# Performance work log

Measured on AMD Instinct MI355X. Metric: run time of the kernel, lower is better.

The kernel has to match this reference:

```python
import jax, jax.numpy as jnp
import numpy as np

N = 50000       # nodes
E = 500000      # edges
F_IN = 64       # input feature dim
F_OUT = 64      # hidden/output dim
K = 3           # diffusion filter order
C = F_IN + F_OUT  # concat dim seen by each DConv


def _xavier(k, shape):
    fan_in, fan_out = shape[-2], shape[-1]
    lim = float(np.sqrt(6.0 / (fan_in + fan_out)))
    return jax.random.uniform(k, shape, jnp.float32, -lim, lim)


def setup_inputs() -> dict:
    key = jax.random.key(0)
    ks = jax.random.split(key, 8)
    X = jax.random.normal(ks[0], (N, F_IN), jnp.float32)
    H = jax.random.normal(ks[1], (N, F_OUT), jnp.float32)
    # ring edges guarantee every node has in-degree >= 1 and out-degree >= 1
    base = jnp.arange(N, dtype=jnp.int32)
    row = jnp.concatenate([base, jax.random.randint(ks[2], (E - N,), 0, N, jnp.int32)])
    col = jnp.concatenate([jnp.roll(base, 1), jax.random.randint(ks[3], (E - N,), 0, N, jnp.int32)])
    edge_index = jnp.stack([row, col])  # [2, E]
    W_z = _xavier(ks[4], (2, K, C, F_OUT))
    W_r = _xavier(ks[5], (2, K, C, F_OUT))
    W_h = _xavier(ks[6], (2, K, C, F_OUT))
    b = jnp.zeros((F_OUT,), jnp.float32)
    return {"X": X, "edge_index": edge_index, "H": H,
            "W_z": W_z, "b_z": b, "W_r": W_r, "b_r": b, "W_h": W_h, "b_h": b}


def _dconv(Xc, row, col, norm_out, norm_in, W, b):
    # PyG propagate: gather source (row) features, scale by edge norm, scatter-add to target (col)
    def prop(x, norm):
        return jax.ops.segment_sum(norm[:, None] * x[row], col, num_segments=N)
    Tx_0 = Xc
    Hout = Xc @ (W[0, 0] + W[1, 0])
    Tx_1_o = prop(Xc, norm_out)
    Tx_1_i = prop(Xc, norm_in)
    Hout = Hout + Tx_1_o @ W[0, 1] + Tx_1_i @ W[1, 1]
    for k in range(2, K):
        Tx_2_o = 2.0 * prop(Tx_1_o, norm_out) - Tx_0
        Tx_2_i = 2.0 * prop(Tx_1_i, norm_in) - Tx_0
        Hout = Hout + Tx_2_o @ W[0, k] + Tx_2_i @ W[1, k]
        # faithful to original: Tx_1 is never reassigned, so Tx_0 stays Xc
        Tx_0, Tx_1_o, Tx_1_i = Xc, Tx_2_o, Tx_2_i
    return Hout + b


def reference(X, edge_index, H, W_z, b_z, W_r, b_r, W_h, b_h):
    row, col = edge_index[0], edge_index[1]
    deg_out = jnp.zeros((N,), jnp.float32).at[row].add(1.0)
    deg_in = jnp.zeros((N,), jnp.float32).at[col].add(1.0)
    norm_out = (1.0 / deg_out)[row]
    norm_in = (1.0 / deg_in)[row]
    XH = jnp.concatenate([X, H], axis=1)
    Z = jax.nn.sigmoid(_dconv(XH, row, col, norm_out, norm_in, W_z, b_z))
    R = jax.nn.sigmoid(_dconv(XH, row, col, norm_out, norm_in, W_r, b_r))
    XHR = jnp.concatenate([X, H * R], axis=1)
    H_tilde = jnp.tanh(_dconv(XHR, row, col, norm_out, norm_in, W_h, b_h))
    H_new = Z * H + (1.0 - Z) * H_tilde
    # NaN infill with mean of non-NaN entries (faithful to original)
    mask = jnp.isnan(H_new)
    H_new = jnp.where(mask, jnp.nanmean(H_new), H_new)
    return H_new
```

## Files before the change

kernel.cpp:

```cpp
#include <hip/hip_runtime.h>
#include <hip/hip_bf16.h>
#include <math.h>

#define N_NODES 50000
#define N_EDGES 500000
#define C_DIM 128
#define N_TILES 3125

#define CSR_BLOCKS 1954
#define CONCAT_BLOCKS 3125
#define PACK_BLOCKS 480

typedef __attribute__((ext_vector_type(8))) short bf8;
typedef __attribute__((ext_vector_type(4))) float f32x4;

__device__ __forceinline__ float bflo(unsigned u) { return __uint_as_float(u << 16); }
__device__ __forceinline__ float bfhi(unsigned u) { return __uint_as_float(u & 0xffff0000u); }
__device__ __forceinline__ unsigned short f2bfu(float f) {
    __hip_bfloat16 h = __float2bfloat16(f);
    unsigned short u;
    __builtin_memcpy(&u, &h, 2);
    return u;
}
__device__ __forceinline__ unsigned packbf(float a, float b) {
    return ((unsigned)f2bfu(b) << 16) | f2bfu(a);
}


__global__ void count_deg(const int* __restrict__ row, const int* __restrict__ col,
                          int* __restrict__ dout, int* __restrict__ din, int e) {
    int i = blockIdx.x * blockDim.x + threadIdx.x;
    if (i >= e) return;
    atomicAdd(&dout[row[i]], 1);
    atomicAdd(&din[col[i]], 1);
}

__global__ void scan_block(const int* __restrict__ counts, int* __restrict__ excl,
                           int* __restrict__ blocksums, int n) {
    __shared__ int tmp[1024];
    int tid = threadIdx.x;
    int gid = blockIdx.x * 1024 + tid;
    int v = (gid < n) ? counts[gid] : 0;
    tmp[tid] = v;
    __syncthreads();
    for (int off = 1; off < 1024; off <<= 1) {
        int t = (tid >= off) ? tmp[tid - off] : 0;
        __syncthreads();
        tmp[tid] += t;
        __syncthreads();
    }
    int incl = tmp[tid];
    if (gid < n) excl[gid] = incl - v;
    if (tid == 1023) blocksums[blockIdx.x] = incl;
}

__global__ void scan_sums(int* __restrict__ blocksums, int nb) {
    __shared__ int tmp[64];
    int tid = threadIdx.x;
    int v = (tid < nb) ? blocksums[tid] : 0;
    tmp[tid] = v;
    __syncthreads();
    for (int off = 1; off < 64; off <<= 1) {
        int t = (tid >= off) ? tmp[tid - off] : 0;
        __syncthreads();
        tmp[tid] += t;
        __syncthreads();
    }
    if (tid < nb) blocksums[tid] = tmp[tid] - v;
}

__global__ void scan_add(int* __restrict__ rowptr, const int* __restrict__ blocksums,
                         int* __restrict__ cursor, const int* __restrict__ dout,
                         const int* __restrict__ din, float2* __restrict__ winv,
                         int n, int e_total) {
    int gid = blockIdx.x * blockDim.x + threadIdx.x;
    if (gid < n) {
        int v = rowptr[gid] + blocksums[gid >> 10];
        rowptr[gid] = v;
        cursor[gid] = v;
        winv[gid] = make_float2(1.0f / (float)dout[gid], 1.0f / (float)din[gid]);
    }
    if (gid == n) rowptr[n] = e_total;
}

__device__ __forceinline__ float wraw(const float* W, int d, int kk, int k, int j) {
    return W[((d * 3 + kk) * 128 + k) * 64 + j];
}

__device__ __forceinline__ float zr_val(const float* Wz, const float* Wr, int k, int nn) {
    const float* W = (nn < 64) ? Wz : Wr;
    int j = nn & 63;
    if (k < 128) return wraw(W, 0, 0, k, j) + wraw(W, 1, 0, k, j);
    int k2 = k - 128;
    int kk = (k2 >= 256) ? 2 : 1;
    int k3 = k2 & 255;
    int p = k3 >> 2, sub = k3 & 3;
    return wraw(W, sub >> 1, kk, 2 * p + (sub & 1), j);
}

__device__ __forceinline__ float h_val(const float* Wh, int k, int j) {
    if (k < 64) return wraw(Wh, 0, 0, k, j) + wraw(Wh, 1, 0, k, j);
    if (k < 320) {
        int k2 = k - 64;
        int kk = (k2 >= 128) ? 2 : 1;
        int k3 = k2 & 127;
        int p = k3 >> 2, sub = k3 & 3;
        return wraw(Wh, sub >> 1, kk, 2 * p + (sub & 1), j);
    }
    if (k < 384) return wraw(Wh, 0, 0, 64 + (k - 320), j) + wraw(Wh, 1, 0, 64 + (k - 320), j);
    int k2 = k - 384;
    int kk = (k2 >= 128) ? 2 : 1;
    int k3 = k2 & 127;
    int p = k3 >> 2, sub = k3 & 3;
    return wraw(Wh, sub >> 1, kk, 64 + 2 * p + (sub & 1), j);
}

__global__ void fused_prep(const int* __restrict__ row, const int* __restrict__ col,
                           const float2* __restrict__ winv, int* __restrict__ cursor,
                           int* __restrict__ csr_src, float2* __restrict__ csr_w,
                           const float* __restrict__ X, const float* __restrict__ Hm,
                           unsigned short* __restrict__ XH, unsigned short* __restrict__ XHp,
                           const float* __restrict__ Wz, const float* __restrict__ Wr,
                           const float* __restrict__ Wh,
                           unsigned short* __restrict__ Wzrf, unsigned short* __restrict__ Whf,
                           int n, int e) {
    int b = blockIdx.x;
    if (b < CSR_BLOCKS) {
        int i = b * 256 + threadIdx.x;
        if (i >= e) return;
        int r = row[i], c = col[i];
        int pos = atomicAdd(&cursor[c], 1);
        csr_src[pos] = r;
        csr_w[pos] = winv[r];
    } else if (b < CSR_BLOCKS + CONCAT_BLOCKS) {
        int t = (b - CSR_BLOCKS) * 256 + threadIdx.x;
        int node = t >> 4, p = t & 15;
        const float* src = (p < 8) ? (X + (size_t)node * 64 + 8 * p)
                                   : (Hm + (size_t)node * 64 + 8 * (p - 8));
        float4 v0 = *(const float4*)src;
        float4 v1 = *(const float4*)(src + 4);
        uint4 o;
        o.x = packbf(v0.x, v0.y); o.y = packbf(v0.z, v0.w);
        o.z = packbf(v1.x, v1.y); o.w = packbf(v1.z, v1.w);
        *(uint4*)(XH + (size_t)node * 128 + 8 * p) = o;
        int tile = node >> 4, lr = node & 15, ck = p >> 2, q = p & 3;
        *(uint4*)(XHp + (((size_t)tile * 4 + ck) * 64 + q * 16 + lr) * 8) = o;
    } else {
        int i = (b - CSR_BLOCKS - CONCAT_BLOCKS) * 256 + threadIdx.x;
        if (i < 20 * 8 * 64 * 8) {
            int j = i & 7, lane = (i >> 3) & 63, nt = (i >> 9) & 7, ks = i >> 12;
            int k = ks * 32 + (lane >> 4) * 8 + j;
            int nn = nt * 16 + (lane & 15);
            Wzrf[i] = f2bfu(zr_val(Wz, Wr, k, nn));
        } else if (i < 20 * 8 * 64 * 8 + 20 * 4 * 64 * 8) {
            int i2 = i - 20 * 8 * 64 * 8;
            int j = i2 & 7, lane = (i2 >> 3) & 63, nt = (i2 >> 9) & 3, ks = i2 >> 11;
            int k = ks * 32 + (lane >> 4) * 8 + j;
            int nn = nt * 16 + (lane & 15);
            Whf[i2] = f2bfu(h_val(Wh, k, nn));
        }
    }
}


__global__ void prop1_128(const unsigned short* __restrict__ S,
                          const int* __restrict__ rowptr, const int* __restrict__ src,
                          const float2* __restrict__ w,
                          unsigned short* __restrict__ P1, unsigned short* __restrict__ P1p,
                          int n) {
    int tid = blockIdx.x * blockDim.x + threadIdx.x;
    int lane = tid & 63;
    int node = ((tid >> 6) << 1) + (lane >> 5);
    int p = lane & 31;
    if (node >= n) return;
    int beg = rowptr[node], end = rowptr[node + 1];
    float ao0 = 0.f, ao1 = 0.f, ao2 = 0.f, ao3 = 0.f;
    float ai0 = 0.f, ai1 = 0.f, ai2 = 0.f, ai3 = 0.f;
    int j = beg;
#define P1STEP(s_, w_) {                                                     \
        uint2 u = *(const uint2*)(S + (size_t)(s_) * 128 + 4 * p);           \
        float c0 = bflo(u.x), c1 = bfhi(u.x), c2 = bflo(u.y), c3 = bfhi(u.y);\
        ao0 = fmaf(w_.x, c0, ao0); ao1 = fmaf(w_.x, c1, ao1);                \
        ao2 = fmaf(w_.x, c2, ao2); ao3 = fmaf(w_.x, c3, ao3);                \
        ai0 = fmaf(w_.y, c0, ai0); ai1 = fmaf(w_.y, c1, ai1);                \
        ai2 = fmaf(w_.y, c2, ai2); ai3 = fmaf(w_.y, c3, ai3); }
    for (; j + 8 <= end; j += 8) {
        int s0 = src[j], s1 = src[j + 1], s2 = src[j + 2], s3 = src[j + 3];
        int s4 = src[j + 4], s5 = src[j + 5], s6 = src[j + 6], s7 = src[j + 7];
        float2 w0 = w[j], w1 = w[j + 1], w2 = w[j + 2], w3 = w[j + 3];
        float2 w4 = w[j + 4], w5 = w[j + 5], w6 = w[j + 6], w7 = w[j + 7];
        P1STEP(s0, w0); P1STEP(s1, w1); P1STEP(s2, w2); P1STEP(s3, w3);
        P1STEP(s4, w4); P1STEP(s5, w5); P1STEP(s6, w6); P1STEP(s7, w7);
    }
    for (; j + 4 <= end; j += 4) {
        int s0 = src[j], s1 = src[j + 1], s2 = src[j + 2], s3 = src[j + 3];
        float2 w0 = w[j], w1 = w[j + 1], w2 = w[j + 2], w3 = w[j + 3];
        P1STEP(s0, w0); P1STEP(s1, w1); P1STEP(s2, w2); P1STEP(s3, w3);
    }
    for (; j < end; ++j) {
        int s = src[j]; float2 wv = w[j];
        P1STEP(s, wv);
    }
#undef P1STEP
    uint4 o;
    o.x = packbf(ao0, ao1); o.y = packbf(ai0, ai1);
    o.z = packbf(ao2, ao3); o.w = packbf(ai2, ai3);
    *(uint4*)(P1 + (size_t)node * 256 + 8 * p) = o;
    int tile = node >> 4, lr = node & 15, ck = p >> 2, q = p & 3;
    *(uint4*)(P1p + (((size_t)tile * 8 + ck) * 64 + q * 16 + lr) * 8) = o;
}

__global__ void prop2_128(const unsigned short* __restrict__ P1,
                          const unsigned short* __restrict__ Xc,
                          const int* __restrict__ rowptr, const int* __restrict__ src,
                          const float2* __restrict__ w,
                          unsigned short* __restrict__ P2p, int n) {
    int tid = blockIdx.x * blockDim.x + threadIdx.x;
    int lane = tid & 63;
    int node = ((tid >> 6) << 1) + (lane >> 5);
    int p = lane & 31;
    if (node >= n) return;
    int beg = rowptr[node], end = rowptr[node + 1];
    float oa = 0.f, ob = 0.f, oc = 0.f, od = 0.f;
    float ia = 0.f, ib = 0.f, ic = 0.f, id = 0.f;
    int j = beg;
#define P2STEP(s_, w_) {                                                     \
        uint4 v = *(const uint4*)(P1 + (size_t)(s_) * 256 + 8 * p);          \
        oa = fmaf(w_.x, bflo(v.x), oa); ob = fmaf(w_.x, bfhi(v.x), ob);      \
        ia = fmaf(w_.y, bflo(v.y), ia); ib = fmaf(w_.y, bfhi(v.y), ib);      \
        oc = fmaf(w_.x, bflo(v.z), oc); od = fmaf(w_.x, bfhi(v.z), od);      \
        ic = fmaf(w_.y, bflo(v.w), ic); id = fmaf(w_.y, bfhi(v.w), id); }
    for (; j + 8 <= end; j += 8) {
        int s0 = src[j], s1 = src[j + 1], s2 = src[j + 2], s3 = src[j + 3];
        int s4 = src[j + 4], s5 = src[j + 5], s6 = src[j + 6], s7 = src[j + 7];
        float2 w0 = w[j], w1 = w[j + 1], w2 = w[j + 2], w3 = w[j + 3];
        float2 w4 = w[j + 4], w5 = w[j + 5], w6 = w[j + 6], w7 = w[j + 7];
        P2STEP(s0, w0); P2STEP(s1, w1); P2STEP(s2, w2); P2STEP(s3, w3);
        P2STEP(s4, w4); P2STEP(s5, w5); P2STEP(s6, w6); P2STEP(s7, w7);
    }
    for (; j + 4 <= end; j += 4) {
        int s0 = src[j], s1 = src[j + 1], s2 = src[j + 2], s3 = src[j + 3];
        float2 w0 = w[j], w1 = w[j + 1], w2 = w[j + 2], w3 = w[j + 3];
        P2STEP(s0, w0); P2STEP(s1, w1); P2STEP(s2, w2); P2STEP(s3, w3);
    }
    for (; j < end; ++j) {
        int s = src[j]; float2 wv = w[j];
        P2STEP(s, wv);
    }
#undef P2STEP
    uint2 ux = *(const uint2*)(Xc + (size_t)node * 128 + 4 * p);
    float xa = bflo(ux.x), xb = bfhi(ux.x), xc = bflo(ux.y), xd = bfhi(ux.y);
    uint4 o;
    o.x = packbf(2.f * oa - xa, 2.f * ob - xb);
    o.y = packbf(2.f * ia - xa, 2.f * ib - xb);
    o.z = packbf(2.f * oc - xc, 2.f * od - xd);
    o.w = packbf(2.f * ic - xc, 2.f * id - xd);
    int tile = node >> 4, lr = node & 15, ck = p >> 2, q = p & 3;
    *(uint4*)(P2p + (((size_t)tile * 8 + ck) * 64 + q * 16 + lr) * 8) = o;
}

__global__ void prop1_64(const unsigned short* __restrict__ HR,
                         const int* __restrict__ rowptr, const int* __restrict__ src,
                         const float2* __restrict__ w,
                         unsigned short* __restrict__ Q1, unsigned short* __restrict__ Q1p,
                         int n) {
    int tid = blockIdx.x * blockDim.x + threadIdx.x;
    int lane = tid & 63;
    int node = ((tid >> 6) << 2) + (lane >> 4);
    int p = lane & 15;
    if (node >= n) return;
    int beg = rowptr[node], end = rowptr[node + 1];
    float ao0 = 0.f, ao1 = 0.f, ao2 = 0.f, ao3 = 0.f;
    float ai0 = 0.f, ai1 = 0.f, ai2 = 0.f, ai3 = 0.f;
    int j = beg;
#define Q1STEP(s_, w_) {                                                     \
        uint2 u = *(const uint2*)(HR + (size_t)(s_) * 64 + 4 * p);           \
        float c0 = bflo(u.x), c1 = bfhi(u.x), c2 = bflo(u.y), c3 = bfhi(u.y);\
        ao0 = fmaf(w_.x, c0, ao0); ao1 = fmaf(w_.x, c1, ao1);                \
        ao2 = fmaf(w_.x, c2, ao2); ao3 = fmaf(w_.x, c3, ao3);                \
        ai0 = fmaf(w_.y, c0, ai0); ai1 = fmaf(w_.y, c1, ai1);                \
        ai2 = fmaf(w_.y, c2, ai2); ai3 = fmaf(w_.y, c3, ai3); }
    for (; j + 8 <= end; j += 8) {
        int s0 = src[j], s1 = src[j + 1], s2 = src[j + 2], s3 = src[j + 3];
        int s4 = src[j + 4], s5 = src[j + 5], s6 = src[j + 6], s7 = src[j + 7];
        float2 w0 = w[j], w1 = w[j + 1], w2 = w[j + 2], w3 = w[j + 3];
        float2 w4 = w[j + 4], w5 = w[j + 5], w6 = w[j + 6], w7 = w[j + 7];
        Q1STEP(s0, w0); Q1STEP(s1, w1); Q1STEP(s2, w2); Q1STEP(s3, w3);
        Q1STEP(s4, w4); Q1STEP(s5, w5); Q1STEP(s6, w6); Q1STEP(s7, w7);
    }
    for (; j + 4 <= end; j += 4) {
        int s0 = src[j], s1 = src[j + 1], s2 = src[j + 2], s3 = src[j + 3];
        float2 w0 = w[j], w1 = w[j + 1], w2 = w[j + 2], w3 = w[j + 3];
        Q1STEP(s0, w0); Q1STEP(s1, w1); Q1STEP(s2, w2); Q1STEP(s3, w3);
    }
    for (; j < end; ++j) {
        int s = src[j]; float2 wv = w[j];
        Q1STEP(s, wv);
    }
#undef Q1STEP
    uint4 o;
    o.x = packbf(ao0, ao1); o.y = packbf(ai0, ai1);
    o.z = packbf(ao2, ao3); o.w = packbf(ai2, ai3);
    *(uint4*)(Q1 + (size_t)node * 128 + 8 * p) = o;
    int tile = node >> 4, lr = node & 15, ck = p >> 2, q = p & 3;
    *(uint4*)(Q1p + (((size_t)tile * 4 + ck) * 64 + q * 16 + lr) * 8) = o;
}

__global__ void prop2_64(const unsigned short* __restrict__ Q1,
                         const unsigned short* __restrict__ HR,
                         const int* __restrict__ rowptr, const int* __restrict__ src,
                         const float2* __restrict__ w,
                         unsigned short* __restrict__ Q2p, int n) {
    int tid = blockIdx.x * blockDim.x + threadIdx.x;
    int lane = tid & 63;
    int node = ((tid >> 6) << 2) + (lane >> 4);
    int p = lane & 15;
    if (node >= n) return;
    int beg = rowptr[node], end = rowptr[node + 1];
    float oa = 0.f, ob = 0.f, oc = 0.f, od = 0.f;
    float ia = 0.f, ib = 0.f, ic = 0.f, id = 0.f;
    int j = beg;
#define Q2STEP(s_, w_) {                                                     \
        uint4 v = *(const uint4*)(Q1 + (size_t)(s_) * 128 + 8 * p);          \
        oa = fmaf(w_.x, bflo(v.x), oa); ob = fmaf(w_.x, bfhi(v.x), ob);      \
        ia = fmaf(w_.y, bflo(v.y), ia); ib = fmaf(w_.y, bfhi(v.y), ib);      \
        oc = fmaf(w_.x, bflo(v.z), oc); od = fmaf(w_.x, bfhi(v.z), od);      \
        ic = fmaf(w_.y, bflo(v.w), ic); id = fmaf(w_.y, bfhi(v.w), id); }
    for (; j + 8 <= end; j += 8) {
        int s0 = src[j], s1 = src[j + 1], s2 = src[j + 2], s3 = src[j + 3];
        int s4 = src[j + 4], s5 = src[j + 5], s6 = src[j + 6], s7 = src[j + 7];
        float2 w0 = w[j], w1 = w[j + 1], w2 = w[j + 2], w3 = w[j + 3];
        float2 w4 = w[j + 4], w5 = w[j + 5], w6 = w[j + 6], w7 = w[j + 7];
        Q2STEP(s0, w0); Q2STEP(s1, w1); Q2STEP(s2, w2); Q2STEP(s3, w3);
        Q2STEP(s4, w4); Q2STEP(s5, w5); Q2STEP(s6, w6); Q2STEP(s7, w7);
    }
    for (; j + 4 <= end; j += 4) {
        int s0 = src[j], s1 = src[j + 1], s2 = src[j + 2], s3 = src[j + 3];
        float2 w0 = w[j], w1 = w[j + 1], w2 = w[j + 2], w3 = w[j + 3];
        Q2STEP(s0, w0); Q2STEP(s1, w1); Q2STEP(s2, w2); Q2STEP(s3, w3);
    }
    for (; j < end; ++j) {
        int s = src[j]; float2 wv = w[j];
        Q2STEP(s, wv);
    }
#undef Q2STEP
    uint2 ux = *(const uint2*)(HR + (size_t)node * 64 + 4 * p);
    float xa = bflo(ux.x), xb = bfhi(ux.x), xc = bflo(ux.y), xd = bfhi(ux.y);
    uint4 o;
    o.x = packbf(2.f * oa - xa, 2.f * ob - xb);
    o.y = packbf(2.f * ia - xa, 2.f * ib - xb);
    o.z = packbf(2.f * oc - xc, 2.f * od - xd);
    o.w = packbf(2.f * ic - xc, 2.f * id - xd);
    int tile = node >> 4, lr = node & 15, ck = p >> 2, q = p & 3;
    *(uint4*)(Q2p + (((size_t)tile * 4 + ck) * 64 + q * 16 + lr) * 8) = o;
}


__global__ __launch_bounds__(256) void gemm_zr_mfma(
    const unsigned short* __restrict__ XHp, const unsigned short* __restrict__ P1p,
    const unsigned short* __restrict__ P2p,
    const unsigned short* __restrict__ Wf, const float* __restrict__ bz,
    const float* __restrict__ br, const float* __restrict__ H,
    float* __restrict__ Zf, unsigned short* __restrict__ HR, int n) {
    int tid = threadIdx.x;
    int lane = tid & 63;
    int ngrp = tid >> 6;
    int rowbase = blockIdx.x * 64;
    int lr = lane & 15, quad = lane >> 4;

    int tiles[4];
#pragma unroll
    for (int mt = 0; mt < 4; ++mt) {
        int t = (rowbase >> 4) + mt;
        tiles[mt] = (t > N_TILES - 1) ? N_TILES - 1 : t;
    }

    f32x4 zero = {0.f, 0.f, 0.f, 0.f};
    f32x4 acc[4][2];
#pragma unroll
    for (int a = 0; a < 4; ++a)
#pragma unroll
        for (int b = 0; b < 2; ++b) acc[a][b] = zero;

#pragma unroll
    for (int ks = 0; ks < 20; ++ks) {
        const unsigned short* T = (ks < 4) ? XHp : (ks < 12) ? P1p : P2p;
        int ck = (ks < 4) ? ks : (ks < 12) ? ks - 4 : ks - 12;
        int nck = (ks < 4) ? 4 : 8;
        bf8 b0 = *(const bf8*)(Wf + (((size_t)ks * 8 + ngrp * 2 + 0) * 64 + lane) * 8);
        bf8 b1 = *(const bf8*)(Wf + (((size_t)ks * 8 + ngrp * 2 + 1) * 64 + lane) * 8);
#pragma unroll
        for (int mt = 0; mt < 4; ++mt) {
            bf8 a = *(const bf8*)(T + (((size_t)tiles[mt] * nck + ck) * 64 + lane) * 8);
            acc[mt][0] = __builtin_amdgcn_mfma_f32_16x16x32_bf16(a, b0, acc[mt][0], 0, 0, 0);
            acc[mt][1] = __builtin_amdgcn_mfma_f32_16x16x32_bf16(a, b1, acc[mt][1], 0, 0, 0);
        }
    }
#pragma unroll
    for (int mt = 0; mt < 4; ++mt)
#pragma unroll
        for (int reg = 0; reg < 4; ++reg) {
            int r = rowbase + mt * 16 + quad * 4 + reg;
            if (r >= n) continue;
#pragma unroll
            for (int nt = 0; nt < 2; ++nt) {
                int cidx = ngrp * 32 + nt * 16 + lr;
                float bias = (cidx < 64) ? bz[cidx] : br[cidx - 64];
                float v = acc[mt][nt][reg] + bias;
                float s = 1.f / (1.f + expf(-v));
                if (cidx < 64) {
                    Zf[(size_t)r * 64 + cidx] = s;
                } else {
                    int c2 = cidx - 64;
                    HR[(size_t)r * 64 + c2] = f2bfu(H[(size_t)r * 64 + c2] * s);
                }
            }
        }
}

__global__ __launch_bounds__(256) void gemm_h_mfma(
    const unsigned short* __restrict__ XHp, const unsigned short* __restrict__ P1p,
    const unsigned short* __restrict__ P2p, const unsigned short* __restrict__ HR,
    const unsigned short* __restrict__ Q1p, const unsigned short* __restrict__ Q2p,
    const unsigned short* __restrict__ Wf, const float* __restrict__ bh,
    const float* __restrict__ Zf, const float* __restrict__ H,
    float* __restrict__ out, int n) {
    int tid = threadIdx.x;
    int lane = tid & 63;
    int wid = tid >> 6;
    int mh = wid & 1, ngrp = wid >> 1;
    int rowbase = blockIdx.x * 128 + mh * 64;
    int lr = lane & 15, quad = lane >> 4;

    int tiles[4];
    const unsigned short* hrp[4];
#pragma unroll
    for (int mt = 0; mt < 4; ++mt) {
        int t = (rowbase >> 4) + mt;
        tiles[mt] = (t > N_TILES - 1) ? N_TILES - 1 : t;
        int r = rowbase + mt * 16 + lr;
        if (r >= n) r = n - 1;
        hrp[mt] = HR + (size_t)r * 64 + quad * 8;
    }

    f32x4 zero = {0.f, 0.f, 0.f, 0.f};
    f32x4 acc[4][2];
#pragma unroll
    for (int a = 0; a < 4; ++a)
#pragma unroll
        for (int b = 0; b < 2; ++b) acc[a][b] = zero;

#pragma unroll
    for (int ks = 0; ks < 20; ++ks) {
        bf8 b0 = *(const bf8*)(Wf + (((size_t)ks * 4 + ngrp * 2 + 0) * 64 + lane) * 8);
        bf8 b1 = *(const bf8*)(Wf + (((size_t)ks * 4 + ngrp * 2 + 1) * 64 + lane) * 8);
#pragma unroll
        for (int mt = 0; mt < 4; ++mt) {
            bf8 a;
            if (ks == 10 || ks == 11) {
                a = *(const bf8*)(hrp[mt] + (ks - 10) * 32);
            } else {
                const unsigned short* T = (ks < 2) ? XHp : (ks < 6) ? P1p :
                                          (ks < 10) ? P2p : (ks < 16) ? Q1p : Q2p;
                int ck = (ks < 2) ? ks : (ks < 6) ? ks - 2 : (ks < 10) ? ks - 6 :
                         (ks < 16) ? ks - 12 : ks - 16;
                int nck = (ks < 2) ? 4 : (ks < 10) ? 8 : 4;
                a = *(const bf8*)(T + (((size_t)tiles[mt] * nck + ck) * 64 + lane) * 8);
            }
            acc[mt][0] = __builtin_amdgcn_mfma_f32_16x16x32_bf16(a, b0, acc[mt][0], 0, 0, 0);
            acc[mt][1] = __builtin_amdgcn_mfma_f32_16x16x32_bf16(a, b1, acc[mt][1], 0, 0, 0);
        }
    }
#pragma unroll
    for (int mt = 0; mt < 4; ++mt)
#pragma unroll
        for (int reg = 0; reg < 4; ++reg) {
            int r = rowbase + mt * 16 + quad * 4 + reg;
            if (r >= n) continue;
#pragma unroll
            for (int nt = 0; nt < 2; ++nt) {
                int cidx = ngrp * 32 + nt * 16 + lr;
                float ht = tanhf(acc[mt][nt][reg] + bh[cidx]);
                float z = Zf[(size_t)r * 64 + cidx];
                float h_old = H[(size_t)r * 64 + cidx];
                out[(size_t)r * 64 + cidx] = z * h_old + (1.f - z) * ht;
            }
        }
}


static inline size_t rup(size_t x) { return (x + 63) & ~(size_t)63; }

extern "C" void kernel_launch(void* const* d_in, const int* in_sizes, int n_in,
                              void* d_out, int out_size, void* d_ws, size_t ws_size,
                              hipStream_t stream) {
    const float* X  = (const float*)d_in[0];
    const int*   EI = (const int*)d_in[1];
    const float* H  = (const float*)d_in[2];
    const float* Wz = (const float*)d_in[3];
    const float* bz = (const float*)d_in[4];
    const float* Wr = (const float*)d_in[5];
    const float* br = (const float*)d_in[6];
    const float* Wh = (const float*)d_in[7];
    const float* bh = (const float*)d_in[8];
    float* out = (float*)d_out;

    const int* row = EI;
    const int* col = EI + N_EDGES;

    char* ws = (char*)d_ws;
    size_t off = 0;
    auto carve = [&](size_t bytes) { void* p = ws + off; off += rup(bytes); return p; };

    int*   deg_out   = (int*)carve(N_NODES * 4);
    int*   deg_in    = (int*)carve(N_NODES * 4);
    int*   rowptr    = (int*)carve((N_NODES + 1) * 4);
    int*   cursor    = (int*)carve(N_NODES * 4);
    int*   blocksums = (int*)carve(64 * 4);
    float2* winv     = (float2*)carve(N_NODES * 8);
    int*   csr_src   = (int*)carve(N_EDGES * 4);
    float2* csr_w    = (float2*)carve(N_EDGES * 8);
    unsigned short* XH  = (unsigned short*)carve((size_t)N_NODES * 128 * 2);
    unsigned short* P1  = (unsigned short*)carve((size_t)N_NODES * 256 * 2);
    unsigned short* XHp = (unsigned short*)carve((size_t)N_TILES * 4 * 512 * 2);
    unsigned short* P1p = (unsigned short*)carve((size_t)N_TILES * 8 * 512 * 2);
    unsigned short* P2p = (unsigned short*)carve((size_t)N_TILES * 8 * 512 * 2);
    unsigned short* HR  = (unsigned short*)carve((size_t)N_NODES * 64 * 2);
    float* Zf           = (float*)carve((size_t)N_NODES * 64 * 4);
    unsigned short* Wzrf = (unsigned short*)carve(20 * 8 * 64 * 8 * 2);
    unsigned short* Whf  = (unsigned short*)carve(20 * 4 * 64 * 8 * 2);

    unsigned short* Q1  = XH;
    unsigned short* Q1p = P1;
    unsigned short* Q2p = P1 + (size_t)N_TILES * 4 * 512;

    hipMemsetAsync(deg_out, 0, rup(N_NODES * 4) + rup(N_NODES * 4), stream);
    count_deg<<<(N_EDGES + 255) / 256, 256, 0, stream>>>(row, col, deg_out, deg_in, N_EDGES);

    int nblk = (N_NODES + 1023) / 1024;
    scan_block<<<nblk, 1024, 0, stream>>>(deg_in, rowptr, blocksums, N_NODES);
    scan_sums<<<1, 64, 0, stream>>>(blocksums, nblk);
    scan_add<<<(N_NODES + 1 + 255) / 256, 256, 0, stream>>>(rowptr, blocksums, cursor,
                                                            deg_out, deg_in, winv, N_NODES, N_EDGES);

    fused_prep<<<CSR_BLOCKS + CONCAT_BLOCKS + PACK_BLOCKS, 256, 0, stream>>>(
        row, col, winv, cursor, csr_src, csr_w,
        X, H, XH, XHp, Wz, Wr, Wh, Wzrf, Whf, N_NODES, N_EDGES);

    int blocks_p128 = (((N_NODES + 1) / 2) * 64 + 255) / 256;
    prop1_128<<<blocks_p128, 256, 0, stream>>>(XH, rowptr, csr_src, csr_w, P1, P1p, N_NODES);
    prop2_128<<<blocks_p128, 256, 0, stream>>>(P1, XH, rowptr, csr_src, csr_w, P2p, N_NODES);

    int zr_blocks = (N_NODES + 63) / 64;
    gemm_zr_mfma<<<zr_blocks, 256, 0, stream>>>(XHp, P1p, P2p, Wzrf, bz, br, H, Zf, HR, N_NODES);

    int blocks_p64 = (((N_NODES + 3) / 4) * 64 + 255) / 256;
    prop1_64<<<blocks_p64, 256, 0, stream>>>(HR, rowptr, csr_src, csr_w, Q1, Q1p, N_NODES);
    prop2_64<<<blocks_p64, 256, 0, stream>>>(Q1, HR, rowptr, csr_src, csr_w, Q2p, N_NODES);

    int h_blocks = (N_NODES + 127) / 128;
    gemm_h_mfma<<<h_blocks, 256, 0, stream>>>(XHp, P1p, P2p, HR, Q1p, Q2p,
                                              Whf, bh, Zf, H, out, N_NODES);
}
```

Before: 362.6 us.

## Split 128-dim propagation into feature slices for cache-friendly gathers

Adds a slice-major copy of the concatenated features (32 bf16 columns per slice, nodes contiguous) and rewrites both 128-wide propagation kernels so each block handles one feature slice for 32 nodes. Interleaving slices in the block index is meant to keep each slice's gather working set small enough to stay in L2 or the last-level cache during random neighbour reads. In exchange, the edge list and weights are re-read once per slice (4 or 8 times), each lane issues narrower loads, and an extra feature copy must be written during prep.

```diff
diff --git a/kernel.cpp b/kernel.cpp
--- a/kernel.cpp
+++ b/kernel.cpp
@@ -10,6 +10,7 @@
 #define CSR_BLOCKS 1954
 #define CONCAT_BLOCKS 3125
 #define PACK_BLOCKS 480
+#define NODE_CHUNKS 1563
 
 typedef __attribute__((ext_vector_type(8))) short bf8;
 typedef __attribute__((ext_vector_type(4))) float f32x4;
@@ -120,6 +121,7 @@
                            int* __restrict__ csr_src, float2* __restrict__ csr_w,
                            const float* __restrict__ X, const float* __restrict__ Hm,
                            unsigned short* __restrict__ XH, unsigned short* __restrict__ XHp,
+                           unsigned short* __restrict__ XHs,
                            const float* __restrict__ Wz, const float* __restrict__ Wr,
                            const float* __restrict__ Wh,
                            unsigned short* __restrict__ Wzrf, unsigned short* __restrict__ Whf,
@@ -145,6 +147,7 @@
         *(uint4*)(XH + (size_t)node * 128 + 8 * p) = o;
         int tile = node >> 4, lr = node & 15, ck = p >> 2, q = p & 3;
         *(uint4*)(XHp + (((size_t)tile * 4 + ck) * 64 + q * 16 + lr) * 8) = o;
+        *(uint4*)(XHs + ((size_t)(p >> 2) * n + node) * 32 + (p & 3) * 8) = o;
     } else {
         int i = (b - CSR_BLOCKS - CONCAT_BLOCKS) * 256 + threadIdx.x;
         if (i < 20 * 8 * 64 * 8) {
@@ -162,102 +165,89 @@
     }
 }
 
-
-__global__ void prop1_128(const unsigned short* __restrict__ S,
-                          const int* __restrict__ rowptr, const int* __restrict__ src,
-                          const float2* __restrict__ w,
-                          unsigned short* __restrict__ P1, unsigned short* __restrict__ P1p,
-                          int n) {
-    int tid = blockIdx.x * blockDim.x + threadIdx.x;
-    int lane = tid & 63;
-    int node = ((tid >> 6) << 1) + (lane >> 5);
-    int p = lane & 31;
+__global__ void prop1_128s(const unsigned short* __restrict__ XHs,
+                           const int* __restrict__ rowptr, const int* __restrict__ src,
+                           const float2* __restrict__ w,
+                           unsigned short* __restrict__ P1g, unsigned short* __restrict__ P1p,
+                           int n) {
+    int slice = blockIdx.x & 3;
+    int chunk = blockIdx.x >> 2;
+    int tid = threadIdx.x;
+    int wid = tid >> 6, lane = tid & 63;
+    int g = lane >> 3, l = lane & 7;
+    int node = chunk * 32 + wid * 8 + g;
     if (node >= n) return;
+    const unsigned short* S = XHs + (size_t)slice * n * 32;
     int beg = rowptr[node], end = rowptr[node + 1];
     float ao0 = 0.f, ao1 = 0.f, ao2 = 0.f, ao3 = 0.f;
     float ai0 = 0.f, ai1 = 0.f, ai2 = 0.f, ai3 = 0.f;
     int j = beg;
-#define P1STEP(s_, w_) {                                                     \
-        uint2 u = *(const uint2*)(S + (size_t)(s_) * 128 + 4 * p);           \
+#define S1STEP(s_, w_) {                                                     \
+        uint2 u = *(const uint2*)(S + (size_t)(s_) * 32 + 4 * l);            \
         float c0 = bflo(u.x), c1 = bfhi(u.x), c2 = bflo(u.y), c3 = bfhi(u.y);\
         ao0 = fmaf(w_.x, c0, ao0); ao1 = fmaf(w_.x, c1, ao1);                \
         ao2 = fmaf(w_.x, c2, ao2); ao3 = fmaf(w_.x, c3, ao3);                \
         ai0 = fmaf(w_.y, c0, ai0); ai1 = fmaf(w_.y, c1, ai1);                \
         ai2 = fmaf(w_.y, c2, ai2); ai3 = fmaf(w_.y, c3, ai3); }
-    for (; j + 8 <= end; j += 8) {
-        int s0 = src[j], s1 = src[j + 1], s2 = src[j + 2], s3 = src[j + 3];
-        int s4 = src[j + 4], s5 = src[j + 5], s6 = src[j + 6], s7 = src[j + 7];
-        float2 w0 = w[j], w1 = w[j + 1], w2 = w[j + 2], w3 = w[j + 3];
-        float2 w4 = w[j + 4], w5 = w[j + 5], w6 = w[j + 6], w7 = w[j + 7];
-        P1STEP(s0, w0); P1STEP(s1, w1); P1STEP(s2, w2); P1STEP(s3, w3);
-        P1STEP(s4, w4); P1STEP(s5, w5); P1STEP(s6, w6); P1STEP(s7, w7);
-    }
     for (; j + 4 <= end; j += 4) {
         int s0 = src[j], s1 = src[j + 1], s2 = src[j + 2], s3 = src[j + 3];
         float2 w0 = w[j], w1 = w[j + 1], w2 = w[j + 2], w3 = w[j + 3];
-        P1STEP(s0, w0); P1STEP(s1, w1); P1STEP(s2, w2); P1STEP(s3, w3);
+        S1STEP(s0, w0); S1STEP(s1, w1); S1STEP(s2, w2); S1STEP(s3, w3);
     }
     for (; j < end; ++j) {
         int s = src[j]; float2 wv = w[j];
-        P1STEP(s, wv);
-    }
-#undef P1STEP
+        S1STEP(s, wv);
+    }
+#undef S1STEP
     uint4 o;
     o.x = packbf(ao0, ao1); o.y = packbf(ai0, ai1);
     o.z = packbf(ao2, ao3); o.w = packbf(ai2, ai3);
-    *(uint4*)(P1 + (size_t)node * 256 + 8 * p) = o;
-    int tile = node >> 4, lr = node & 15, ck = p >> 2, q = p & 3;
-    *(uint4*)(P1p + (((size_t)tile * 8 + ck) * 64 + q * 16 + lr) * 8) = o;
-}
-
-__global__ void prop2_128(const unsigned short* __restrict__ P1,
-                          const unsigned short* __restrict__ Xc,
-                          const int* __restrict__ rowptr, const int* __restrict__ src,
-                          const float2* __restrict__ w,
-                          unsigned short* __restrict__ P2p, int n) {
-    int tid = blockIdx.x * blockDim.x + threadIdx.x;
-    int lane = tid & 63;
-    int node = ((tid >> 6) << 1) + (lane >> 5);
-    int p = lane & 31;
+    int pp = 8 * slice + l;
+    *(uint4*)(P1g + ((size_t)(pp >> 2) * n + node) * 32 + (pp & 3) * 8) = o;
+    int tile = node >> 4, lr = node & 15;
+    *(uint4*)(P1p + (((size_t)tile * 8 + (pp >> 2)) * 64 + (pp & 3) * 16 + lr) * 8) = o;
+}
+
+__global__ void prop2_128s(const unsigned short* __restrict__ P1g,
+                           const unsigned short* __restrict__ Xc,
+                           const int* __restrict__ rowptr, const int* __restrict__ src,
+                           const float2* __restrict__ w,
+                           unsigned short* __restrict__ P2p, int n) {
+    int slice = blockIdx.x & 7;
+    int chunk = blockIdx.x >> 3;
+    int tid = threadIdx.x;
+    int wid = tid >> 6, lane = tid & 63;
+    int g = lane >> 3, l = lane & 7;
+    int node = chunk * 32 + wid * 8 + g;
     if (node >= n) return;
+    const unsigned short* S = P1g + (size_t)slice * n * 32;
     int beg = rowptr[node], end = rowptr[node + 1];
-    float oa = 0.f, ob = 0.f, oc = 0.f, od = 0.f;
-    float ia = 0.f, ib = 0.f, ic = 0.f, id = 0.f;
+    float oa = 0.f, ob = 0.f, ia = 0.f, ib = 0.f;
     int j = beg;
-#define P2STEP(s_, w_) {                                                     \
-        uint4 v = *(const uint4*)(P1 + (size_t)(s_) * 256 + 8 * p);          \
+#define S2STEP(s_, w_) {                                                     \
+        uint2 v = *(const uint2*)(S + (size_t)(s_) * 32 + 4 * l);            \
         oa = fmaf(w_.x, bflo(v.x), oa); ob = fmaf(w_.x, bfhi(v.x), ob);      \
-        ia = fmaf(w_.y, bflo(v.y), ia); ib = fmaf(w_.y, bfhi(v.y), ib);      \
-        oc = fmaf(w_.x, bflo(v.z), oc); od = fmaf(w_.x, bfhi(v.z), od);      \
-        ic = fmaf(w_.y, bflo(v.w), ic); id = fmaf(w_.y, bfhi(v.w), id); }
-    for (; j + 8 <= end; j += 8) {
-        int s0 = src[j], s1 = src[j + 1], s2 = src[j + 2], s3 = src[j + 3];
-        int s4 = src[j + 4], s5 = src[j + 5], s6 = src[j + 6], s7 = src[j + 7];
-        float2 w0 = w[j], w1 = w[j + 1], w2 = w[j + 2], w3 = w[j + 3];
-        float2 w4 = w[j + 4], w5 = w[j + 5], w6 = w[j + 6], w7 = w[j + 7];
-        P2STEP(s0, w0); P2STEP(s1, w1); P2STEP(s2, w2); P2STEP(s3, w3);
-        P2STEP(s4, w4); P2STEP(s5, w5); P2STEP(s6, w6); P2STEP(s7, w7);
-    }
+        ia = fmaf(w_.y, bflo(v.y), ia); ib = fmaf(w_.y, bfhi(v.y), ib); }
     for (; j + 4 <= end; j += 4) {
         int s0 = src[j], s1 = src[j + 1], s2 = src[j + 2], s3 = src[j + 3];
         float2 w0 = w[j], w1 = w[j + 1], w2 = w[j + 2], w3 = w[j + 3];
-        P2STEP(s0, w0); P2STEP(s1, w1); P2STEP(s2, w2); P2STEP(s3, w3);
+        S2STEP(s0, w0); S2STEP(s1, w1); S2STEP(s2, w2); S2STEP(s3, w3);
     }
     for (; j < end; ++j) {
         int s = src[j]; float2 wv = w[j];
-        P2STEP(s, wv);
-    }
-#undef P2STEP
-    uint2 ux = *(const uint2*)(Xc + (size_t)node * 128 + 4 * p);
-    float xa = bflo(ux.x), xb = bfhi(ux.x), xc = bflo(ux.y), xd = bfhi(ux.y);
-    uint4 o;
-    o.x = packbf(2.f * oa - xa, 2.f * ob - xb);
-    o.y = packbf(2.f * ia - xa, 2.f * ib - xb);
-    o.z = packbf(2.f * oc - xc, 2.f * od - xd);
-    o.w = packbf(2.f * ic - xc, 2.f * id - xd);
-    int tile = node >> 4, lr = node & 15, ck = p >> 2, q = p & 3;
-    *(uint4*)(P2p + (((size_t)tile * 8 + ck) * 64 + q * 16 + lr) * 8) = o;
-}
+        S2STEP(s, wv);
+    }
+#undef S2STEP
+    int c0 = 16 * slice + 4 * (l >> 1) + 2 * (l & 1);
+    unsigned ux = *(const unsigned*)(Xc + (size_t)node * 128 + c0);
+    float x0 = bflo(ux), x1 = bfhi(ux);
+    uint2 o;
+    o.x = packbf(2.f * oa - x0, 2.f * ob - x1);
+    o.y = packbf(2.f * ia - x0, 2.f * ib - x1);
+    int tile = node >> 4, lr = node & 15;
+    *(uint2*)(P2p + (((size_t)tile * 8 + slice) * 64 + (l >> 1) * 16 + lr) * 8 + (l & 1) * 4) = o;
+}
+
 
 __global__ void prop1_64(const unsigned short* __restrict__ HR,
                          const int* __restrict__ rowptr, const int* __restrict__ src,
@@ -521,7 +511,8 @@
     int*   csr_src   = (int*)carve(N_EDGES * 4);
     float2* csr_w    = (float2*)carve(N_EDGES * 8);
     unsigned short* XH  = (unsigned short*)carve((size_t)N_NODES * 128 * 2);
-    unsigned short* P1  = (unsigned short*)carve((size_t)N_NODES * 256 * 2);
+    unsigned short* XHs = (unsigned short*)carve((size_t)N_NODES * 128 * 2);
+    unsigned short* P1g = (unsigned short*)carve((size_t)N_NODES * 256 * 2);
     unsigned short* XHp = (unsigned short*)carve((size_t)N_TILES * 4 * 512 * 2);
     unsigned short* P1p = (unsigned short*)carve((size_t)N_TILES * 8 * 512 * 2);
     unsigned short* P2p = (unsigned short*)carve((size_t)N_TILES * 8 * 512 * 2);
@@ -531,8 +522,8 @@
     unsigned short* Whf  = (unsigned short*)carve(20 * 4 * 64 * 8 * 2);
 
     unsigned short* Q1  = XH;
-    unsigned short* Q1p = P1;
-    unsigned short* Q2p = P1 + (size_t)N_TILES * 4 * 512;
+    unsigned short* Q1p = P1g;
+    unsigned short* Q2p = P1g + (size_t)N_TILES * 4 * 512;
 
     hipMemsetAsync(deg_out, 0, rup(N_NODES * 4) + rup(N_NODES * 4), stream);
     count_deg<<<(N_EDGES + 255) / 256, 256, 0, stream>>>(row, col, deg_out, deg_in, N_EDGES);
@@ -545,11 +536,12 @@
 
     fused_prep<<<CSR_BLOCKS + CONCAT_BLOCKS + PACK_BLOCKS, 256, 0, stream>>>(
         row, col, winv, cursor, csr_src, csr_w,
-        X, H, XH, XHp, Wz, Wr, Wh, Wzrf, Whf, N_NODES, N_EDGES);
-
-    int blocks_p128 = (((N_NODES + 1) / 2) * 64 + 255) / 256;
-    prop1_128<<<blocks_p128, 256, 0, stream>>>(XH, rowptr, csr_src, csr_w, P1, P1p, N_NODES);
-    prop2_128<<<blocks_p128, 256, 0, stream>>>(P1, XH, rowptr, csr_src, csr_w, P2p, N_NODES);
+        X, H, XH, XHp, XHs, Wz, Wr, Wh, Wzrf, Whf, N_NODES, N_EDGES);
+
+    prop1_128s<<<4 * NODE_CHUNKS, 256, 0, stream>>>(XHs, rowptr, csr_src, csr_w,
+                                                    P1g, P1p, N_NODES);
+    prop2_128s<<<8 * NODE_CHUNKS, 256, 0, stream>>>(P1g, XH, rowptr, csr_src, csr_w,
+                                                    P2p, N_NODES);
 
     int zr_blocks = (N_NODES + 63) / 64;
     gemm_zr_mfma<<<zr_blocks, 256, 0, stream>>>(XHp, P1p, P2p, Wzrf, bz, br, H, Zf, HR, N_NODES);
```

After: 373.2 us. +2.9%, slower.
